# Kernel optimization log

Hardware: AMD Instinct MI355X
Metric: run time of the kernel (lower is better)

## Reference

```python
import jax, jax.numpy as jnp
import numpy as np

S, B, D, H, F = 2048, 4, 256, 8, 2048
HD = D // H


def _ln(x, g, b, eps=1e-5):
    mu = jnp.mean(x, axis=-1, keepdims=True)
    var = jnp.var(x, axis=-1, keepdims=True)
    return (x - mu) * jax.lax.rsqrt(var + eps) * g + b


def setup_inputs() -> dict:
    key = jax.random.key(0)
    ks = jax.random.split(key, 8)
    s = lambda fan: 1.0 / np.sqrt(fan)
    return {
        "features": jax.random.normal(ks[0], (S, B, D), jnp.float32),
        "ln_g": jnp.ones((D,), jnp.float32),
        "ln_b": jnp.zeros((D,), jnp.float32),
        "in_proj_w": jax.random.normal(ks[1], (3 * D, D), jnp.float32) * s(D),
        "in_proj_b": jnp.zeros((3 * D,), jnp.float32),
        "out_proj_w": jax.random.normal(ks[2], (D, D), jnp.float32) * s(D),
        "out_proj_b": jnp.zeros((D,), jnp.float32),
        "w1": jax.random.normal(ks[3], (F, D), jnp.float32) * s(D),
        "b1": jnp.zeros((F,), jnp.float32),
        "w2": jax.random.normal(ks[4], (D, F), jnp.float32) * s(F),
        "b2": jnp.zeros((D,), jnp.float32),
    }


def _attn_tanh_relu(x, in_proj_w, in_proj_b, out_proj_w, out_proj_b):
    # x: (S, B, D). Standard MHA projections, but relu(tanh(.)) replaces softmax.
    qkv = x @ in_proj_w.T + in_proj_b            # (S, B, 3D)
    q, k, v = jnp.split(qkv, 3, axis=-1)
    q = q.reshape(S, B, H, HD) * (1.0 / np.sqrt(HD))
    k = k.reshape(S, B, H, HD)
    v = v.reshape(S, B, H, HD)
    scores = jnp.einsum("sbhd,tbhd->bhst", q, k)  # (B, H, S, S)
    w = jax.nn.relu(jnp.tanh(scores))
    out = jnp.einsum("bhst,tbhd->sbhd", w, v).reshape(S, B, D)
    return out @ out_proj_w.T + out_proj_b


def reference(features, ln_g, ln_b, in_proj_w, in_proj_b, out_proj_w, out_proj_b, w1, b1, w2, b2):
    ln_x = _ln(features, ln_g, ln_b)
    attn = _attn_tanh_relu(ln_x, in_proj_w, in_proj_b, out_proj_w, out_proj_b)
    r1 = _ln(ln_x + attn, ln_g, ln_b)
    ff = jax.nn.relu(r1 @ w1.T + b1) @ w2.T + b2
    return _ln(r1 + ff, ln_g, ln_b)
```

## Files before the change

kernel.cpp:

```cpp
#include <hip/hip_runtime.h>
#include <hip/hip_bf16.h>

#define SS 2048
#define BB 4
#define DD 256
#define HH 8
#define HDD 32
#define FFD 2048
#define MM (SS*BB)

typedef __attribute__((ext_vector_type(8))) __bf16 bf16x8;
typedef __attribute__((ext_vector_type(2))) __bf16 bf16x2;
typedef __attribute__((ext_vector_type(8))) short short8;
typedef __attribute__((ext_vector_type(4))) short short4v;
typedef __attribute__((ext_vector_type(4))) float f32x4;
typedef __attribute__((ext_vector_type(16))) float f32x16;
typedef __attribute__((ext_vector_type(2))) unsigned uint2v;
typedef __attribute__((ext_vector_type(4))) unsigned uint4v;

__device__ __forceinline__ unsigned short f2bf(float f) {
  union { float f; unsigned u; } v; v.f = f;
  unsigned r = v.u + 0x7fffu + ((v.u >> 16) & 1u);
  return (unsigned short)(r >> 16);
}

__device__ __forceinline__ float bf2f(short s) {
  union { float f; unsigned u; } v;
  v.u = ((unsigned)(unsigned short)s) << 16;
  return v.f;
}

__device__ __forceinline__ unsigned pk2(float a, float b) {
  bf16x2 t; t[0] = (__bf16)a; t[1] = (__bf16)b;
  return __builtin_bit_cast(unsigned, t);
}

__device__ __forceinline__ void gload16(const void* g, void* l) {
  __builtin_amdgcn_global_load_lds(
      (const __attribute__((address_space(1))) void*)g,
      (__attribute__((address_space(3))) void*)l, 16, 0, 0);
}

__global__ __launch_bounds__(256)
void cvt_ln(const float* __restrict__ a, const float* __restrict__ b,
            const float* __restrict__ c, const float* __restrict__ d,
            short* __restrict__ oa, short* __restrict__ ob,
            short* __restrict__ oc, short* __restrict__ od,
            const float* __restrict__ feat,
            const float* __restrict__ gam, const float* __restrict__ bet,
            float* __restrict__ lnf, short* __restrict__ lnb)
{
  if (blockIdx.y == 1) {
    const int bx = blockIdx.x;
    if (bx >= 1280) return;
    const float* in; short* out; int i;
    if (bx < 192)      { in = a; out = oa; i = bx * 256 + threadIdx.x; }
    else if (bx < 256) { in = b; out = ob; i = (bx - 192) * 256 + threadIdx.x; }
    else if (bx < 768) { in = c; out = oc; i = (bx - 256) * 256 + threadIdx.x; }
    else               { in = d; out = od; i = (bx - 768) * 256 + threadIdx.x; }
    float4 x = ((const float4*)in)[i];
    short4v o = { (short)f2bf(x.x), (short)f2bf(x.y), (short)f2bf(x.z), (short)f2bf(x.w) };
    ((short4v*)out)[i] = o;
    return;
  }
  const int w = threadIdx.x >> 6, l = threadIdx.x & 63;
  const size_t row = (size_t)blockIdx.x * 4 + w;
  float4 x = *(const float4*)&feat[row * 256 + l * 4];
  float sum = x.x + x.y + x.z + x.w;
  float sq  = x.x*x.x + x.y*x.y + x.z*x.z + x.w*x.w;
#pragma unroll
  for (int off = 32; off > 0; off >>= 1) {
    sum += __shfl_xor(sum, off);
    sq  += __shfl_xor(sq, off);
  }
  const float mu = sum * (1.f / 256.f);
  const float rs = rsqrtf(sq * (1.f / 256.f) - mu * mu + 1e-5f);
  const float4 g4 = *(const float4*)&gam[l * 4];
  const float4 b4 = *(const float4*)&bet[l * 4];
  const float y0 = (x.x - mu) * rs * g4.x + b4.x;
  const float y1 = (x.y - mu) * rs * g4.y + b4.y;
  const float y2 = (x.z - mu) * rs * g4.z + b4.z;
  const float y3 = (x.w - mu) * rs * g4.w + b4.w;
  float4 o; o.x = y0; o.y = y1; o.z = y2; o.w = y3;
  *(float4*)&lnf[row * 256 + l * 4] = o;
  short4v ob2 = { (short)f2bf(y0), (short)f2bf(y1), (short)f2bf(y2), (short)f2bf(y3) };
  *(short4v*)&lnb[row * 256 + l * 4] = ob2;
}

template<int NIN, int WF, int WBF, int BFI>
__global__ __launch_bounds__(256)
void ln_kernel(const float* __restrict__ xa, const void* __restrict__ xb,
               const void* __restrict__ xc,
               const float* __restrict__ gam, const float* __restrict__ bet,
               float* __restrict__ outf, short* __restrict__ outb)
{
  const int w = threadIdx.x >> 6, l = threadIdx.x & 63;
  const size_t row = (size_t)blockIdx.x * 4 + w;
  float4 x = *(const float4*)&xa[row * 256 + l * 4];
  if (NIN >= 2) {
    if (BFI) {
      const short4v yb = *(const short4v*)&((const short*)xb)[row * 256 + l * 4];
      x.x += bf2f(yb[0]); x.y += bf2f(yb[1]); x.z += bf2f(yb[2]); x.w += bf2f(yb[3]);
    } else {
      const float4 yv = *(const float4*)&((const float*)xb)[row * 256 + l * 4];
      x.x += yv.x; x.y += yv.y; x.z += yv.z; x.w += yv.w;
    }
  }
  if (NIN >= 3) {
    if (BFI) {
      const short4v yc = *(const short4v*)&((const short*)xc)[row * 256 + l * 4];
      x.x += bf2f(yc[0]); x.y += bf2f(yc[1]); x.z += bf2f(yc[2]); x.w += bf2f(yc[3]);
    } else {
      const float4 yv = *(const float4*)&((const float*)xc)[row * 256 + l * 4];
      x.x += yv.x; x.y += yv.y; x.z += yv.z; x.w += yv.w;
    }
  }
  float sum = x.x + x.y + x.z + x.w;
  float sq  = x.x*x.x + x.y*x.y + x.z*x.z + x.w*x.w;
#pragma unroll
  for (int off = 32; off > 0; off >>= 1) {
    sum += __shfl_xor(sum, off);
    sq  += __shfl_xor(sq, off);
  }
  const float mu = sum * (1.f / 256.f);
  const float rs = rsqrtf(sq * (1.f / 256.f) - mu * mu + 1e-5f);
  const float4 g4 = *(const float4*)&gam[l * 4];
  const float4 b4 = *(const float4*)&bet[l * 4];
  const float y0 = (x.x - mu) * rs * g4.x + b4.x;
  const float y1 = (x.y - mu) * rs * g4.y + b4.y;
  const float y2 = (x.z - mu) * rs * g4.z + b4.z;
  const float y3 = (x.w - mu) * rs * g4.w + b4.w;
  if (WF) {
    float4 o; o.x = y0; o.y = y1; o.z = y2; o.w = y3;
    *(float4*)&outf[row * 256 + l * 4] = o;
  }
  if (WBF) {
    short4v o = { (short)f2bf(y0), (short)f2bf(y1), (short)f2bf(y2), (short)f2bf(y3) };
    *(short4v*)&outb[row * 256 + l * 4] = o;
  }
}

template<int EPI, int BM, int BN, int KW>
__global__ __launch_bounds__(256)
void gemm_bt(const short* __restrict__ A, const short* __restrict__ W,
             const float* __restrict__ bias, void* __restrict__ out,
             void* __restrict__ out2, int K, int N, int Ksub)
{
  __shared__ short sA[2][BM * 64];
  __shared__ short sB[2][BN * 64];
  const int tid = threadIdx.x;
  const int l  = tid & 63;
  const int w  = tid >> 6;
  const int wr = w >> 1, wc = w & 1;
  const int lr = l & 15, lg = l >> 4;
  const long row0 = (long)blockIdx.y * BM;
  const long col0 = (long)blockIdx.x * BN;
  const int kz = blockIdx.z;
  const int kbeg = kz * Ksub;
  const int ldsw = (tid & ~63) * 16;
  constexpr int MR = BM / 32, NR = BN / 32;
  f32x4 acc[MR][NR] = {};
  const int nt = Ksub / 64;

  auto stage = [&](int buf, int k0) {
#pragma unroll
    for (int i = 0; i < BM / 32; i++) {
      const int o = (i * 256 + tid) * 16;
      const int r = o >> 7;
      const int cg = ((o >> 4) & 7) ^ (r & 7);
      gload16((const char*)A + ((row0 + r) * (long)K + k0) * 2 + cg * 16,
              (char*)sA[buf] + i * 4096 + ldsw);
    }
    const long wstride = KW ? KW : K;
    const long wk = KW ? (k0 & (KW - 1)) : k0;
#pragma unroll
    for (int i = 0; i < BN / 32; i++) {
      const int o = (i * 256 + tid) * 16;
      const int r = o >> 7;
      const int cg = ((o >> 4) & 7) ^ (r & 7);
      gload16((const char*)W + ((col0 + r) * wstride + wk) * 2 + cg * 16,
              (char*)sB[buf] + i * 4096 + ldsw);
    }
  };

  stage(0, kbeg);
  __syncthreads();
  int cur = 0;
  for (int t = 0; t < nt; t++) {
    if (t + 1 < nt) stage(cur ^ 1, kbeg + (t + 1) * 64);
    bf16x8 af[MR][2], bw[NR][2];
#pragma unroll
    for (int m = 0; m < MR; m++)
#pragma unroll
      for (int kk = 0; kk < 2; kk++) {
        const int row = wr * (BM/2) + m * 16 + lr;
        af[m][kk] = *(const bf16x8*)&sA[cur][row * 64 + (((kk*4 + lg) ^ (lr & 7)) * 8)];
      }
#pragma unroll
    for (int n = 0; n < NR; n++)
#pragma unroll
      for (int kk = 0; kk < 2; kk++) {
        const int row = wc * (BN/2) + n * 16 + lr;
        bw[n][kk] = *(const bf16x8*)&sB[cur][row * 64 + (((kk*4 + lg) ^ (lr & 7)) * 8)];
      }
#pragma unroll
    for (int kk = 0; kk < 2; kk++)
#pragma unroll
      for (int m = 0; m < MR; m++)
#pragma unroll
        for (int n = 0; n < NR; n++)
          acc[m][n] = __builtin_amdgcn_mfma_f32_16x16x32_bf16(af[m][kk], bw[n][kk], acc[m][n], 0, 0, 0);
    __syncthreads();
    cur ^= 1;
  }

#pragma unroll
  for (int m = 0; m < MR; m++) {
    const long rbase = row0 + wr * (BM/2) + m * 16 + lg * 4;
#pragma unroll
    for (int n = 0; n < NR; n++) {
      const long c = col0 + wc * (BN/2) + n * 16 + lr;
      const float bv = (EPI == 3 && kz) ? 0.f : bias[c];
#pragma unroll
      for (int j = 0; j < 4; j++) {
        const long r = rbase + j;
        float val = acc[m][n][j] + bv;
        if (EPI == 0) {
          const int part = (int)(c >> 8);
          const int cc = (int)(c & 255);
          const int h = cc >> 5, hd = cc & 31;
          const int bi = (int)(r & 3);
          const int s = (int)(r >> 2);
          const int bh = bi * HH + h;
          if (part == 0) val *= 0.51006972771029396f;
          size_t idx;
          if (part == 2) {
            idx = (size_t)2 * (MM * DD) + (size_t)bh * (SS * HDD)
                + (size_t)(s >> 3) * (HDD * 8) + hd * 8 + (s & 7);
          } else {
            idx = (size_t)part * (MM * DD) + ((size_t)bh * SS + s) * HDD + hd;
          }
          ((short*)out)[idx] = (short)f2bf(val);
        } else if (EPI == 2) {
          ((short*)out)[(size_t)r * N + c] = (short)f2bf(fmaxf(val, 0.f));
        } else if (EPI == 3) {
          short* op = kz ? (short*)out2 : (short*)out;
          op[(size_t)r * N + c] = (short)f2bf(val);
        } else {
          ((short*)out)[(size_t)r * N + c] = (short)f2bf(val);
        }
      }
    }
  }
}

__global__ __launch_bounds__(512, 4)
void attn_kernel(const short* __restrict__ Qb, const short* __restrict__ Kb,
                 const short* __restrict__ Vb, short* __restrict__ Aout)
{
  const int tid = threadIdx.x;
  const int l = tid & 63, w = tid >> 6;
  const int q32 = l & 31, hf = l >> 5;
  const int i = blockIdx.x;
  const int j = i >> 3;
  const int p = (i & 7) + 8 * (j >> 3);
  const int q0 = (j & 7) * 256 + w * 32;
  const size_t base = (size_t)p * SS * HDD;
  const short* Q  = Qb + base;
  const short* Kp = Kb + base;
  const short* Vp = Vb + base;

  const short* qrow = &Q[(size_t)(q0 + q32) * HDD];
  const bf16x8 qf0 = *(const bf16x8*)&qrow[hf * 8];
  const bf16x8 qf1 = *(const bf16x8*)&qrow[16 + hf * 8];

  const f32x16 fzero = {};
  f32x16 accA = {}, accB = {};

  auto loadK = [&](int t0, bf16x8* kf) {
    const short* kr = &Kp[(size_t)(t0 + q32) * HDD];
    kf[0] = *(const bf16x8*)&kr[hf * 8];
    kf[1] = *(const bf16x8*)&kr[16 + hf * 8];
  };
  auto loadV = [&](int t0, bf16x8* vf) {
    const short* vb = &Vp[(size_t)((t0 >> 3) + hf) * (HDD * 8) + q32 * 8];
    vf[0] = *(const bf16x8*)&vb[0];
    vf[1] = *(const bf16x8*)&vb[2 * (HDD * 8)];
  };

  auto step = [&](const bf16x8* kf, const bf16x8* vf, f32x16& acc) {
    f32x16 s = __builtin_amdgcn_mfma_f32_32x32x16_bf16(kf[0], qf0, fzero, 0, 0, 0);
    s = __builtin_amdgcn_mfma_f32_32x32x16_bf16(kf[1], qf1, s, 0, 0, 0);
    float pv[16];
#pragma unroll
    for (int r = 0; r < 16; r++) {
      const float e = __builtin_amdgcn_exp2f(s[r]);
      pv[r] = fmaxf(1.f - 2.f * __builtin_amdgcn_rcpf(e + 1.f), 0.f);
    }
    unsigned X0 = pk2(pv[0], pv[1]),   X1 = pk2(pv[2], pv[3]);
    unsigned X2 = pk2(pv[4], pv[5]),   X3 = pk2(pv[6], pv[7]);
    unsigned X4 = pk2(pv[8], pv[9]),   X5 = pk2(pv[10], pv[11]);
    unsigned X6 = pk2(pv[12], pv[13]), X7 = pk2(pv[14], pv[15]);
    uint2v r02 = __builtin_amdgcn_permlane32_swap(X0, X2, false, false);
    uint2v r13 = __builtin_amdgcn_permlane32_swap(X1, X3, false, false);
    uint2v r46 = __builtin_amdgcn_permlane32_swap(X4, X6, false, false);
    uint2v r57 = __builtin_amdgcn_permlane32_swap(X5, X7, false, false);
    const uint4v f0 = { r02[0], r13[0], r02[1], r13[1] };
    const uint4v f1 = { r46[0], r57[0], r46[1], r57[1] };
    const bf16x8 pa0 = __builtin_bit_cast(bf16x8, f0);
    const bf16x8 pa1 = __builtin_bit_cast(bf16x8, f1);
    acc = __builtin_amdgcn_mfma_f32_32x32x16_bf16(pa0, vf[0], acc, 0, 0, 0);
    acc = __builtin_amdgcn_mfma_f32_32x32x16_bf16(pa1, vf[1], acc, 0, 0, 0);
  };

  bf16x8 kA[2], vA[2], kB[2], vB[2];
  loadK(0, kA); loadV(0, vA);
  for (int t0 = 0; t0 < SS; t0 += 64) {
    loadK(t0 + 32, kB); loadV(t0 + 32, vB);
    step(kA, vA, accA);
    const int tn = (t0 + 64 < SS) ? t0 + 64 : 0;
    loadK(tn, kA); loadV(tn, vA);
    step(kB, vB, accB);
  }

  const int bi = p >> 3, hh = p & 7;
  const size_t colo = (size_t)hh * HDD + q32;
#pragma unroll
  for (int r = 0; r < 16; r++) {
    const int crow = (r & 3) + 8 * (r >> 2) + 4 * hf;
    Aout[((size_t)(q0 + crow) * BB + bi) * DD + colo] =
        (short)f2bf(accA[r] + accB[r]);
  }
}

extern "C" void kernel_launch(void* const* d_in, const int* in_sizes, int n_in,
                              void* d_out, int out_size, void* d_ws, size_t ws_size,
                              hipStream_t stream) {
  const float* features   = (const float*)d_in[0];
  const float* ln_g       = (const float*)d_in[1];
  const float* ln_b       = (const float*)d_in[2];
  const float* in_proj_w  = (const float*)d_in[3];
  const float* in_proj_b  = (const float*)d_in[4];
  const float* out_proj_w = (const float*)d_in[5];
  const float* out_proj_b = (const float*)d_in[6];
  const float* w1 = (const float*)d_in[7];
  const float* b1 = (const float*)d_in[8];
  const float* w2 = (const float*)d_in[9];
  const float* b2 = (const float*)d_in[10];

  char* ws = (char*)d_ws;
  const size_t MB = 1024 * 1024;
  float* lnx_f  = (float*)(ws + 0);
  short* lnx_b  = (short*)(ws + 8 * MB);
  short* qkv    = (short*)(ws + 12 * MB);
  short* aprt   = (short*)(ws + 24 * MB);
  short* proj   = (short*)(ws + 12 * MB);
  short* r1_b   = (short*)(ws + 20 * MB);
  float* r1_f   = (float*)(ws + 24 * MB);
  short* h1     = (short*)(ws + 32 * MB);
  short* ffb    = (short*)(ws + 12 * MB);
  short* ffp1   = (short*)(ws + 16 * MB);
  short* wqkv_b = (short*)(ws + 64 * MB);
  short* wout_b = wqkv_b + 768 * 256;
  short* w1_b   = wout_b + 256 * 256;
  short* w2_b   = w1_b + 2048 * 256;

  cvt_ln<<<dim3(2048, 2), 256, 0, stream>>>(in_proj_w, out_proj_w, w1, w2,
                                            wqkv_b, wout_b, w1_b, w2_b,
                                            features, ln_g, ln_b, lnx_f, lnx_b);

  gemm_bt<0, 128, 64, 0><<<dim3(12, 64, 1), 256, 0, stream>>>(lnx_b, wqkv_b, in_proj_b, qkv, nullptr, 256, 768, 256);

  attn_kernel<<<dim3(256, 1, 1), 512, 0, stream>>>(qkv, qkv + 2097152, qkv + 2 * 2097152, aprt);

  gemm_bt<4, 64, 64, 0><<<dim3(4, 128, 1), 256, 0, stream>>>(aprt, wout_b, out_proj_b, proj, nullptr, 256, 256, 256);

  ln_kernel<2, 1, 1, 1><<<2048, 256, 0, stream>>>(lnx_f, proj, nullptr, ln_g, ln_b, r1_f, r1_b);

  gemm_bt<2, 128, 128, 0><<<dim3(16, 64, 1), 256, 0, stream>>>(r1_b, w1_b, b1, h1, nullptr, 256, 2048, 256);

  gemm_bt<3, 128, 64, 0><<<dim3(4, 64, 2), 256, 0, stream>>>(h1, w2_b, b2, ffb, ffp1, 2048, 256, 1024);

  ln_kernel<3, 1, 0, 1><<<2048, 256, 0, stream>>>(r1_f, ffb, ffp1, ln_g, ln_b, (float*)d_out, nullptr);
}
```

Baseline: 124.7 us.

## Drop fp32 residual copies; fold residual into FFN2 epilogue and use bf16 LN inputs

The first LayerNorm no longer writes an fp32 copy, and the middle LayerNorm reads the bf16 ln_x and projection and writes only a bf16 r1. The residual r1 is added inside the split-K FFN2 GEMM epilogue on the kz==0 slice, so the final LayerNorm sums just two bf16 partial buffers. This cuts fp32 traffic in several memory-bound kernels and reshuffles the workspace layout. In exchange, the residual stream is carried in bf16 instead of fp32, which lowers accuracy.

```diff
diff --git a/kernel.cpp b/kernel.cpp
--- a/kernel.cpp
+++ b/kernel.cpp
@@ -48,7 +48,7 @@
             short* __restrict__ oc, short* __restrict__ od,
             const float* __restrict__ feat,
             const float* __restrict__ gam, const float* __restrict__ bet,
-            float* __restrict__ lnf, short* __restrict__ lnb)
+            short* __restrict__ lnb)
 {
   if (blockIdx.y == 1) {
     const int bx = blockIdx.x;
@@ -77,44 +77,28 @@
   const float rs = rsqrtf(sq * (1.f / 256.f) - mu * mu + 1e-5f);
   const float4 g4 = *(const float4*)&gam[l * 4];
   const float4 b4 = *(const float4*)&bet[l * 4];
-  const float y0 = (x.x - mu) * rs * g4.x + b4.x;
-  const float y1 = (x.y - mu) * rs * g4.y + b4.y;
-  const float y2 = (x.z - mu) * rs * g4.z + b4.z;
-  const float y3 = (x.w - mu) * rs * g4.w + b4.w;
-  float4 o; o.x = y0; o.y = y1; o.z = y2; o.w = y3;
-  *(float4*)&lnf[row * 256 + l * 4] = o;
-  short4v ob2 = { (short)f2bf(y0), (short)f2bf(y1), (short)f2bf(y2), (short)f2bf(y3) };
+  short4v ob2 = { (short)f2bf((x.x - mu) * rs * g4.x + b4.x),
+                  (short)f2bf((x.y - mu) * rs * g4.y + b4.y),
+                  (short)f2bf((x.z - mu) * rs * g4.z + b4.z),
+                  (short)f2bf((x.w - mu) * rs * g4.w + b4.w) };
   *(short4v*)&lnb[row * 256 + l * 4] = ob2;
 }
 
-template<int NIN, int WF, int WBF, int BFI>
+template<int WF, int WBF>
 __global__ __launch_bounds__(256)
-void ln_kernel(const float* __restrict__ xa, const void* __restrict__ xb,
-               const void* __restrict__ xc,
-               const float* __restrict__ gam, const float* __restrict__ bet,
-               float* __restrict__ outf, short* __restrict__ outb)
+void ln2bf(const short* __restrict__ xa, const short* __restrict__ xb,
+           const float* __restrict__ gam, const float* __restrict__ bet,
+           float* __restrict__ outf, short* __restrict__ outb)
 {
   const int w = threadIdx.x >> 6, l = threadIdx.x & 63;
   const size_t row = (size_t)blockIdx.x * 4 + w;
-  float4 x = *(const float4*)&xa[row * 256 + l * 4];
-  if (NIN >= 2) {
-    if (BFI) {
-      const short4v yb = *(const short4v*)&((const short*)xb)[row * 256 + l * 4];
-      x.x += bf2f(yb[0]); x.y += bf2f(yb[1]); x.z += bf2f(yb[2]); x.w += bf2f(yb[3]);
-    } else {
-      const float4 yv = *(const float4*)&((const float*)xb)[row * 256 + l * 4];
-      x.x += yv.x; x.y += yv.y; x.z += yv.z; x.w += yv.w;
-    }
-  }
-  if (NIN >= 3) {
-    if (BFI) {
-      const short4v yc = *(const short4v*)&((const short*)xc)[row * 256 + l * 4];
-      x.x += bf2f(yc[0]); x.y += bf2f(yc[1]); x.z += bf2f(yc[2]); x.w += bf2f(yc[3]);
-    } else {
-      const float4 yv = *(const float4*)&((const float*)xc)[row * 256 + l * 4];
-      x.x += yv.x; x.y += yv.y; x.z += yv.z; x.w += yv.w;
-    }
-  }
+  const short4v ya = *(const short4v*)&xa[row * 256 + l * 4];
+  const short4v yb = *(const short4v*)&xb[row * 256 + l * 4];
+  float4 x;
+  x.x = bf2f(ya[0]) + bf2f(yb[0]);
+  x.y = bf2f(ya[1]) + bf2f(yb[1]);
+  x.z = bf2f(ya[2]) + bf2f(yb[2]);
+  x.w = bf2f(ya[3]) + bf2f(yb[3]);
   float sum = x.x + x.y + x.z + x.w;
   float sq  = x.x*x.x + x.y*x.y + x.z*x.z + x.w*x.w;
 #pragma unroll
@@ -144,7 +128,8 @@
 __global__ __launch_bounds__(256)
 void gemm_bt(const short* __restrict__ A, const short* __restrict__ W,
              const float* __restrict__ bias, void* __restrict__ out,
-             void* __restrict__ out2, int K, int N, int Ksub)
+             void* __restrict__ out2, const short* __restrict__ resid,
+             int K, int N, int Ksub)
 {
   __shared__ short sA[2][BM * 64];
   __shared__ short sB[2][BN * 64];
@@ -244,6 +229,7 @@
         } else if (EPI == 2) {
           ((short*)out)[(size_t)r * N + c] = (short)f2bf(fmaxf(val, 0.f));
         } else if (EPI == 3) {
+          if (kz == 0) val += bf2f(resid[(size_t)r * N + c]);
           short* op = kz ? (short*)out2 : (short*)out;
           op[(size_t)r * N + c] = (short)f2bf(val);
         } else {
@@ -350,16 +336,14 @@
 
   char* ws = (char*)d_ws;
   const size_t MB = 1024 * 1024;
-  float* lnx_f  = (float*)(ws + 0);
+  short* ffb    = (short*)(ws + 0);
+  short* ffp1   = (short*)(ws + 4 * MB);
   short* lnx_b  = (short*)(ws + 8 * MB);
   short* qkv    = (short*)(ws + 12 * MB);
+  short* r1_b   = (short*)(ws + 12 * MB);
+  short* proj   = (short*)(ws + 16 * MB);
   short* aprt   = (short*)(ws + 24 * MB);
-  short* proj   = (short*)(ws + 12 * MB);
-  short* r1_b   = (short*)(ws + 20 * MB);
-  float* r1_f   = (float*)(ws + 24 * MB);
   short* h1     = (short*)(ws + 32 * MB);
-  short* ffb    = (short*)(ws + 12 * MB);
-  short* ffp1   = (short*)(ws + 16 * MB);
   short* wqkv_b = (short*)(ws + 64 * MB);
   short* wout_b = wqkv_b + 768 * 256;
   short* w1_b   = wout_b + 256 * 256;
@@ -367,19 +351,19 @@
 
   cvt_ln<<<dim3(2048, 2), 256, 0, stream>>>(in_proj_w, out_proj_w, w1, w2,
                                             wqkv_b, wout_b, w1_b, w2_b,
-                                            features, ln_g, ln_b, lnx_f, lnx_b);
-
-  gemm_bt<0, 128, 64, 0><<<dim3(12, 64, 1), 256, 0, stream>>>(lnx_b, wqkv_b, in_proj_b, qkv, nullptr, 256, 768, 256);
+                                            features, ln_g, ln_b, lnx_b);
+
+  gemm_bt<0, 128, 64, 0><<<dim3(12, 64, 1), 256, 0, stream>>>(lnx_b, wqkv_b, in_proj_b, qkv, nullptr, nullptr, 256, 768, 256);
 
   attn_kernel<<<dim3(256, 1, 1), 512, 0, stream>>>(qkv, qkv + 2097152, qkv + 2 * 2097152, aprt);
 
-  gemm_bt<4, 64, 64, 0><<<dim3(4, 128, 1), 256, 0, stream>>>(aprt, wout_b, out_proj_b, proj, nullptr, 256, 256, 256);
-
-  ln_kernel<2, 1, 1, 1><<<2048, 256, 0, stream>>>(lnx_f, proj, nullptr, ln_g, ln_b, r1_f, r1_b);
-
-  gemm_bt<2, 128, 128, 0><<<dim3(16, 64, 1), 256, 0, stream>>>(r1_b, w1_b, b1, h1, nullptr, 256, 2048, 256);
-
-  gemm_bt<3, 128, 64, 0><<<dim3(4, 64, 2), 256, 0, stream>>>(h1, w2_b, b2, ffb, ffp1, 2048, 256, 1024);
-
-  ln_kernel<3, 1, 0, 1><<<2048, 256, 0, stream>>>(r1_f, ffb, ffp1, ln_g, ln_b, (float*)d_out, nullptr);
-}
+  gemm_bt<4, 64, 64, 0><<<dim3(4, 128, 1), 256, 0, stream>>>(aprt, wout_b, out_proj_b, proj, nullptr, nullptr, 256, 256, 256);
+
+  ln2bf<0, 1><<<2048, 256, 0, stream>>>(lnx_b, proj, ln_g, ln_b, nullptr, r1_b);
+
+  gemm_bt<2, 128, 128, 0><<<dim3(16, 64, 1), 256, 0, stream>>>(r1_b, w1_b, b1, h1, nullptr, nullptr, 256, 2048, 256);
+
+  gemm_bt<3, 128, 64, 0><<<dim3(4, 64, 2), 256, 0, stream>>>(h1, w2_b, b2, ffb, ffp1, r1_b, 2048, 256, 1024);
+
+  ln2bf<1, 0><<<2048, 256, 0, stream>>>(ffb, ffp1, ln_g, ln_b, (float*)d_out, nullptr);
+}
```

Measured after the change: 126.5 us. No clear change (+1.4%).
